# Kernel tuning notes

Measured on AMD Instinct MI355X. Metric: run time of the kernel, lower is better.

## Reference

```python
import jax, jax.numpy as jnp
import numpy as np

IN_CH = 256
OUT_CH = 256
LATENT = 512
SCALE = 1.0 / IN_CH ** 0.5


def setup_inputs() -> dict:
    key = jax.random.key(0)
    k1, k2, k3, k4 = jax.random.split(key, 4)
    return {
        "x": jax.random.normal(k1, (16, IN_CH, 64, 64), dtype=jnp.float32),
        "w": jax.random.normal(k2, (16, LATENT), dtype=jnp.float32),
        "style_w": jax.random.normal(k3, (IN_CH, LATENT), dtype=jnp.float32) * (1.0 / LATENT ** 0.5),
        "style_b": jnp.zeros((IN_CH,), dtype=jnp.float32),
        "weight": jax.random.normal(k4, (1, OUT_CH, IN_CH, 3, 3), dtype=jnp.float32),
    }


def reference(x, w, style_w, style_b, weight):
    b, c, h, ws = x.shape
    # style = Linear(latent -> in_channels), reshaped to [b,1,in,1,1]
    style = (w @ style_w.T + style_b)[:, None, :, None, None]
    wt = weight * SCALE                    # [1, O, I, 3, 3]
    wt = wt * (style + 1.0)                # [b, O, I, 3, 3]
    demod = jax.lax.rsqrt(jnp.sum(wt * wt, axis=(2, 3, 4), keepdims=True) + 1e-8)
    wt = wt * demod
    # grouped conv: fold batch into channels, groups = b
    x2 = x.reshape(1, b * c, h, ws)
    k = wt.reshape(b * OUT_CH, c, 3, 3)
    out = jax.lax.conv_general_dilated(
        x2, k,
        window_strides=(1, 1),
        padding=((1, 1), (1, 1)),
        dimension_numbers=("NCHW", "OIHW", "NCHW"),
        feature_group_count=b,
    )
    return out.reshape(b, OUT_CH, h, ws)
```

## Files before the change

kernel.cpp:

```cpp
#include <hip/hip_runtime.h>
#include <hip/hip_bf16.h>

#define IN_CH 256
#define OUT_CH 256
#define LATENT 512
#define MSCALE (1.0f / 16.0f)

typedef __attribute__((ext_vector_type(8)))  short bf16x8;
typedef __attribute__((ext_vector_type(16))) float f32x16;
typedef unsigned short u16;

__device__ __forceinline__ u16 f2bf(float f) {
  unsigned int x = __float_as_uint(f);
  x += 0x7fffu + ((x >> 16) & 1u);
  return (u16)(x >> 16);
}

__device__ __forceinline__ void gload_lds16(const u16* g, u16* l) {
#if defined(__has_builtin) && __has_builtin(__builtin_amdgcn_global_load_lds)
  __builtin_amdgcn_global_load_lds(
      (const __attribute__((address_space(1))) unsigned int*)g,
      (__attribute__((address_space(3))) unsigned int*)l, 16, 0, 0);
#else
  int lane = __builtin_amdgcn_mbcnt_hi(~0u, __builtin_amdgcn_mbcnt_lo(~0u, 0));
  ((uint4*)l)[lane] = *(const uint4*)g;
#endif
}

__global__ void k_prep(const float* __restrict__ weight, const float* __restrict__ w,
                       const float* __restrict__ sw, const float* __restrict__ sb,
                       float* __restrict__ wsq, u16* __restrict__ wb,
                       float* __restrict__ mod) {
  const int bid = blockIdx.x, tid = threadIdx.x;
  if (bid < 256) {
    const int o = bid, i = tid;
    const float* wp = weight + ((size_t)o * IN_CH + i) * 9;
    float s = 0.f;
#pragma unroll
    for (int t = 0; t < 9; ++t) {
      float v = wp[t];
      s += v * v;
      wb[(((size_t)t * 32 + (i >> 3)) * OUT_CH + o) * 8 + (i & 7)] = f2bf(v);
    }
    wsq[o * IN_CH + i] = s;
  } else {
    __shared__ float ws[LATENT];
    const int b = bid - 256;
    ws[tid] = w[b * LATENT + tid];
    ws[tid + 256] = w[b * LATENT + 256 + tid];
    __syncthreads();
    const float4* sr = (const float4*)(sw + (size_t)tid * LATENT);
    const float4* wr = (const float4*)ws;
    float s = 0.f;
#pragma unroll 8
    for (int l = 0; l < LATENT / 4; ++l) {
      float4 a = sr[l], c = wr[l];
      s += a.x * c.x + a.y * c.y + a.z * c.z + a.w * c.w;
    }
    mod[b * IN_CH + tid] = (1.0f + s + sb[tid]) * MSCALE;
  }
}

__global__ void k_pad(const float* __restrict__ x, const float* __restrict__ mod,
                      const float* __restrict__ wsq, u16* __restrict__ xs,
                      float* __restrict__ demod) {
  const int bid = blockIdx.x;
  const int b = bid / 66, pr = bid - b * 66;
  const int tid = threadIdx.x;
  u16* rowbase = xs + (size_t)((b * 66 + pr) * 32) * 528;

  if (pr == 0 || pr == 65) {
    uint4 z = {0, 0, 0, 0};
    uint4* p = (uint4*)rowbase;
#pragma unroll
    for (int it = 0; it < 9; ++it) {
      int idx = it * 256 + tid;
      if (idx < 2112) p[idx] = z;
    }
    if (pr == 0) {
      __shared__ float m2[IN_CH];
      float m = mod[b * IN_CH + tid];
      m2[tid] = m * m;
      __syncthreads();
      float s = 1e-8f;
      const float4* wr = (const float4*)(wsq + (size_t)tid * IN_CH);
      const float4* mq = (const float4*)m2;
#pragma unroll 4
      for (int i = 0; i < IN_CH / 4; ++i) {
        float4 a = wr[i], c = mq[i];
        s += a.x * c.x + a.y * c.y + a.z * c.z + a.w * c.w;
      }
      demod[b * OUT_CH + tid] = rsqrtf(s);
    }
    return;
  }

  __shared__ float modsh[IN_CH];
  modsh[tid] = mod[b * IN_CH + tid];
  __syncthreads();

  const int w = tid & 63, Gq = tid >> 6;
  const int h = pr - 1;
  const float* xrow = x + ((size_t)b * IN_CH * 64 + (size_t)h) * 64 + w;

  if (tid < 64) {
    bf16x8 z = {};
    *(bf16x8*)(rowbase + ((size_t)(tid >> 1) * 66 + (tid & 1) * 65) * 8) = z;
  }
#pragma unroll
  for (int it = 0; it < 8; ++it) {
    const int G = it * 4 + Gq;
    const float* p = xrow + (size_t)G * 8 * 4096;
    bf16x8 q;
#pragma unroll
    for (int j = 0; j < 8; ++j)
      q[j] = (short)f2bf(p[(size_t)j * 4096] * modsh[G * 8 + j]);
    *(bf16x8*)(rowbase + ((size_t)G * 66 + (w + 1)) * 8) = q;
  }
}

__global__ __launch_bounds__(256, 2)
void k_conv(const u16* __restrict__ xs, const u16* __restrict__ wb,
            const float* __restrict__ demod, float* __restrict__ out) {
  __shared__ __align__(16) u16 xlds[2 * 10 * 2 * 66 * 8];
  __shared__ __align__(16) u16 wlds[2 * 9 * 2 * 64 * 8];

  const int tid = threadIdx.x;
  const int lane = tid & 63;
  const int wid = tid >> 6;
  const int ol = lane & 31;
  const int hi = lane >> 5;

  const int bid = blockIdx.x;
  const int sbid = ((bid & 7) << 6) | (bid >> 3);
  const int otile = (sbid & 3) << 6;
  const int hbase = ((sbid >> 2) & 7) << 3;
  const int b = sbid >> 5;

  const u16* xsb = xs + (size_t)((b * 66 + hbase) * 32) * 528;

  int xoff[5];
#pragma unroll
  for (int it = 0; it < 5; ++it) {
    int q = it * 256 + tid;
    int r = q / 132, rem = q - r * 132;
    int g = rem / 66, c = rem - g * 66;
    xoff[it] = (r * 32 + g) * 528 + c * 8;
  }
  const int xofft = (9 * 32 + 1) * 528 + (26 + tid) * 8;
  int woff[4];
#pragma unroll
  for (int it = 0; it < 4; ++it) {
    int p = it * 256 + tid;
    int t = p >> 7, g = (p >> 6) & 1, o = p & 63;
    woff[it] = ((t * 32 + g) * OUT_CH + otile + o) * 8;
  }
  const int wofft = ((8 * 32 + ((tid >> 6) & 1)) * OUT_CH + otile + (tid & 63)) * 8;

  auto stage = [&](int buf, int ic) {
    const int ibx = ic * 1056;
    const int ibw = ic * 4096;
    u16* xd = xlds + buf * 10560;
#pragma unroll
    for (int it = 0; it < 5; ++it)
      gload_lds16(xsb + xoff[it] + ibx, xd + (size_t)(it * 256 + wid * 64) * 8);
    if (tid < 40)
      gload_lds16(xsb + xofft + ibx, xd + (size_t)(1280 + wid * 64) * 8);
    u16* wd = wlds + buf * 9216;
#pragma unroll
    for (int it = 0; it < 4; ++it)
      gload_lds16(wb + woff[it] + ibw, wd + (size_t)(it * 256 + wid * 64) * 8);
    if (tid < 128)
      gload_lds16(wb + wofft + ibw, wd + (size_t)(1024 + wid * 64) * 8);
  };

  f32x16 acc[2][4] = {};

  stage(0, 0);
  __syncthreads();

  for (int ic = 0; ic < 16; ++ic) {
    const int buf = ic & 1;
    const u16* xp = xlds + buf * 10560;
    const u16* wp = wlds + buf * 9216;

    if (ic < 15) stage(buf ^ 1, ic + 1);

    bf16x8 Xc[2][6];
#pragma unroll
    for (int rr = 0; rr < 2; ++rr)
#pragma unroll
      for (int ch = 0; ch < 2; ++ch)
#pragma unroll
        for (int dw = 0; dw < 3; ++dw) {
          const int r = 2 * wid + 1 + rr;
          const int c = ch * 32 + ol + dw;
          Xc[rr][ch * 3 + dw] = *(const bf16x8*)(xp + (size_t)((r * 2 + hi) * 66 + c) * 8);
        }

    __builtin_amdgcn_s_setprio(1);
#pragma unroll
    for (int dh = 0; dh < 3; ++dh) {
      bf16x8 A0[3], A1[3];
#pragma unroll
      for (int dw = 0; dw < 3; ++dw) {
        const int t = dh * 3 + dw;
        A0[dw] = *(const bf16x8*)(wp + (size_t)((t * 2 + hi) * 64 + ol) * 8);
        A1[dw] = *(const bf16x8*)(wp + (size_t)((t * 2 + hi) * 64 + 32 + ol) * 8);
      }
#pragma unroll
      for (int dw = 0; dw < 3; ++dw) {
#pragma unroll
        for (int ps = 0; ps < 4; ++ps) {
          const int rowoff = ps >> 1, ch = ps & 1;
          const int rl = rowoff + dh;
          bf16x8 B;
          if (rl == 0 || rl == 3) {
            const int r = 2 * wid + rl;
            const int c = ch * 32 + ol + dw;
            B = *(const bf16x8*)(xp + (size_t)((r * 2 + hi) * 66 + c) * 8);
          } else {
            B = Xc[rl - 1][ch * 3 + dw];
          }
          acc[0][ps] = __builtin_amdgcn_mfma_f32_32x32x16_bf16(A0[dw], B, acc[0][ps], 0, 0, 0);
          acc[1][ps] = __builtin_amdgcn_mfma_f32_32x32x16_bf16(A1[dw], B, acc[1][ps], 0, 0, 0);
        }
      }
    }
    __builtin_amdgcn_s_setprio(0);
    __syncthreads();
  }

  const float* dmb = demod + b * OUT_CH + otile;
  float* outb = out + (size_t)b * OUT_CH * 4096;
#pragma unroll
  for (int os = 0; os < 2; ++os) {
    float dm[16];
#pragma unroll
    for (int qd = 0; qd < 4; ++qd) {
      float4 d4 = *(const float4*)(dmb + os * 32 + qd * 8 + hi * 4);
      dm[qd * 4 + 0] = d4.x; dm[qd * 4 + 1] = d4.y;
      dm[qd * 4 + 2] = d4.z; dm[qd * 4 + 3] = d4.w;
    }
#pragma unroll
    for (int ps = 0; ps < 4; ++ps) {
      const int prow = hbase + 2 * wid + (ps >> 1);
      const int col = (ps & 1) * 32 + ol;
#pragma unroll
      for (int rr = 0; rr < 16; ++rr) {
        const int orow = (rr & 3) + 8 * (rr >> 2) + 4 * hi;
        const int o = otile + os * 32 + orow;
        outb[(size_t)o * 4096 + prow * 64 + col] = acc[os][ps][rr] * dm[rr];
      }
    }
  }
}

extern "C" void kernel_launch(void* const* d_in, const int* in_sizes, int n_in,
                              void* d_out, int out_size, void* d_ws, size_t ws_size,
                              hipStream_t stream) {
  const float* x  = (const float*)d_in[0];
  const float* w  = (const float*)d_in[1];
  const float* sw = (const float*)d_in[2];
  const float* sb = (const float*)d_in[3];
  const float* wt = (const float*)d_in[4];
  float* out = (float*)d_out;

  char* ws = (char*)d_ws;
  u16*   xs    = (u16*)(ws);
  u16*   wbuf  = (u16*)(ws + 35684352);
  float* mod   = (float*)(ws + 36864000);
  float* demod = (float*)(ws + 36880384);
  float* wsq   = (float*)(ws + 36896768);
  if (ws_size < 37158912u) return;

  k_prep<<<272, 256, 0, stream>>>(wt, w, sw, sb, wsq, wbuf, mod);
  k_pad <<<16 * 66, 256, 0, stream>>>(x, mod, wsq, xs, demod);
  k_conv<<<512, 256, 0, stream>>>(xs, wbuf, demod, out);
}
```

Baseline: 105.4 us.

## Halve conv tile height, single-buffer X tile, raise occupancy to three blocks

The conv block now covers 4 output rows instead of 8, so there are twice as many blocks. Each warp accumulates one row instead of two, which halves the accumulator registers and drops the cached X rows. The X tile in LDS is single-buffered, staged after a barrier at the end of each iteration, while the weights stay double-buffered. Launch bounds are raised to 3 blocks per SM and demod is cached in LDS. The aim is more resident waves to hide latency, at the cost of less weight reuse per block, more halo reloads, and X loads that are no longer overlapped with compute.

```diff
diff --git a/kernel.cpp b/kernel.cpp
--- a/kernel.cpp
+++ b/kernel.cpp
@@ -119,11 +119,12 @@
   }
 }
 
-__global__ __launch_bounds__(256, 2)
+__global__ __launch_bounds__(256, 3)
 void k_conv(const u16* __restrict__ xs, const u16* __restrict__ wb,
             const float* __restrict__ demod, float* __restrict__ out) {
-  __shared__ __align__(16) u16 xlds[2 * 10 * 2 * 66 * 8];
+  __shared__ __align__(16) u16 xlds[6 * 2 * 66 * 8];
   __shared__ __align__(16) u16 wlds[2 * 9 * 2 * 64 * 8];
+  __shared__ __align__(16) float dmsh[64];
 
   const int tid = threadIdx.x;
   const int lane = tid & 63;
@@ -132,41 +133,47 @@
   const int hi = lane >> 5;
 
   const int bid = blockIdx.x;
-  const int sbid = ((bid & 7) << 6) | (bid >> 3);
+  const int sbid = ((bid & 7) << 7) | (bid >> 3);
   const int otile = (sbid & 3) << 6;
-  const int hbase = ((sbid >> 2) & 7) << 3;
-  const int b = sbid >> 5;
-
-  const u16* xsb = xs + (size_t)((b * 66 + hbase) * 32) * 528;
-
-  int xoff[5];
-#pragma unroll
-  for (int it = 0; it < 5; ++it) {
+  const int hb = ((sbid >> 2) & 15) << 2;
+  const int b = sbid >> 6;
+
+  const u16* xsb = xs + (size_t)((b * 66 + hb) * 32) * 528;
+
+  int xoff[3];
+#pragma unroll
+  for (int it = 0; it < 3; ++it) {
     int q = it * 256 + tid;
     int r = q / 132, rem = q - r * 132;
     int g = rem / 66, c = rem - g * 66;
     xoff[it] = (r * 32 + g) * 528 + c * 8;
   }
-  const int xofft = (9 * 32 + 1) * 528 + (26 + tid) * 8;
+  int xofft;
+  {
+    int q = 768 + tid;
+    int r = q / 132, rem = q - r * 132;
+    int g = rem / 66, c = rem - g * 66;
+    xofft = (r * 32 + g) * 528 + c * 8;
+  }
   int woff[4];
 #pragma unroll
   for (int it = 0; it < 4; ++it) {
-    int p = it * 256 + tid;
-    int t = p >> 7, g = (p >> 6) & 1, o = p & 63;
+    int q = it * 256 + tid;
+    int t = q >> 7, g = (q >> 6) & 1, o = q & 63;
     woff[it] = ((t * 32 + g) * OUT_CH + otile + o) * 8;
   }
   const int wofft = ((8 * 32 + ((tid >> 6) & 1)) * OUT_CH + otile + (tid & 63)) * 8;
 
-  auto stage = [&](int buf, int ic) {
+  auto stageX = [&](int ic) {
     const int ibx = ic * 1056;
+#pragma unroll
+    for (int it = 0; it < 3; ++it)
+      gload_lds16(xsb + xoff[it] + ibx, xlds + (size_t)(it * 256 + wid * 64) * 8);
+    if (tid < 24)
+      gload_lds16(xsb + xofft + ibx, xlds + (size_t)(768 + wid * 64) * 8);
+  };
+  auto stageW = [&](int ic, u16* wd) {
     const int ibw = ic * 4096;
-    u16* xd = xlds + buf * 10560;
-#pragma unroll
-    for (int it = 0; it < 5; ++it)
-      gload_lds16(xsb + xoff[it] + ibx, xd + (size_t)(it * 256 + wid * 64) * 8);
-    if (tid < 40)
-      gload_lds16(xsb + xofft + ibx, xd + (size_t)(1280 + wid * 64) * 8);
-    u16* wd = wlds + buf * 9216;
 #pragma unroll
     for (int it = 0; it < 4; ++it)
       gload_lds16(wb + woff[it] + ibw, wd + (size_t)(it * 256 + wid * 64) * 8);
@@ -174,83 +181,58 @@
       gload_lds16(wb + wofft + ibw, wd + (size_t)(1024 + wid * 64) * 8);
   };
 
-  f32x16 acc[2][4] = {};
-
-  stage(0, 0);
+  f32x16 acc[2][2] = {};
+
+  if (tid < 64) dmsh[tid] = demod[b * OUT_CH + otile + tid];
+  stageX(0);
+  stageW(0, wlds);
   __syncthreads();
 
   for (int ic = 0; ic < 16; ++ic) {
-    const int buf = ic & 1;
-    const u16* xp = xlds + buf * 10560;
-    const u16* wp = wlds + buf * 9216;
-
-    if (ic < 15) stage(buf ^ 1, ic + 1);
-
-    bf16x8 Xc[2][6];
-#pragma unroll
-    for (int rr = 0; rr < 2; ++rr)
-#pragma unroll
-      for (int ch = 0; ch < 2; ++ch)
-#pragma unroll
-        for (int dw = 0; dw < 3; ++dw) {
-          const int r = 2 * wid + 1 + rr;
-          const int c = ch * 32 + ol + dw;
-          Xc[rr][ch * 3 + dw] = *(const bf16x8*)(xp + (size_t)((r * 2 + hi) * 66 + c) * 8);
-        }
+    const u16* wp = wlds + (ic & 1) * 9216;
+    if (ic < 15) stageW(ic + 1, wlds + ((ic & 1) ^ 1) * 9216);
 
     __builtin_amdgcn_s_setprio(1);
 #pragma unroll
-    for (int dh = 0; dh < 3; ++dh) {
-      bf16x8 A0[3], A1[3];
-#pragma unroll
-      for (int dw = 0; dw < 3; ++dw) {
-        const int t = dh * 3 + dw;
-        A0[dw] = *(const bf16x8*)(wp + (size_t)((t * 2 + hi) * 64 + ol) * 8);
-        A1[dw] = *(const bf16x8*)(wp + (size_t)((t * 2 + hi) * 64 + 32 + ol) * 8);
+    for (int t = 0; t < 9; ++t) {
+      const int dh = t / 3, dw = t - dh * 3;
+      bf16x8 A0 = *(const bf16x8*)(wp + (size_t)((t * 2 + hi) * 64 + ol) * 8);
+      bf16x8 A1 = *(const bf16x8*)(wp + (size_t)((t * 2 + hi) * 64 + 32 + ol) * 8);
+#pragma unroll
+      for (int ch = 0; ch < 2; ++ch) {
+        const int rl = wid + dh;
+        const int c = ch * 32 + ol + dw;
+        bf16x8 B = *(const bf16x8*)(xlds + (size_t)((rl * 2 + hi) * 66 + c) * 8);
+        acc[0][ch] = __builtin_amdgcn_mfma_f32_32x32x16_bf16(A0, B, acc[0][ch], 0, 0, 0);
+        acc[1][ch] = __builtin_amdgcn_mfma_f32_32x32x16_bf16(A1, B, acc[1][ch], 0, 0, 0);
       }
-#pragma unroll
-      for (int dw = 0; dw < 3; ++dw) {
-#pragma unroll
-        for (int ps = 0; ps < 4; ++ps) {
-          const int rowoff = ps >> 1, ch = ps & 1;
-          const int rl = rowoff + dh;
-          bf16x8 B;
-          if (rl == 0 || rl == 3) {
-            const int r = 2 * wid + rl;
-            const int c = ch * 32 + ol + dw;
-            B = *(const bf16x8*)(xp + (size_t)((r * 2 + hi) * 66 + c) * 8);
-          } else {
-            B = Xc[rl - 1][ch * 3 + dw];
-          }
-          acc[0][ps] = __builtin_amdgcn_mfma_f32_32x32x16_bf16(A0[dw], B, acc[0][ps], 0, 0, 0);
-          acc[1][ps] = __builtin_amdgcn_mfma_f32_32x32x16_bf16(A1[dw], B, acc[1][ps], 0, 0, 0);
-        }
-      }
     }
     __builtin_amdgcn_s_setprio(0);
+
+    __builtin_amdgcn_s_barrier();
+    if (ic < 15) stageX(ic + 1);
     __syncthreads();
   }
 
-  const float* dmb = demod + b * OUT_CH + otile;
   float* outb = out + (size_t)b * OUT_CH * 4096;
+  const int prow = hb + wid;
 #pragma unroll
   for (int os = 0; os < 2; ++os) {
     float dm[16];
 #pragma unroll
     for (int qd = 0; qd < 4; ++qd) {
-      float4 d4 = *(const float4*)(dmb + os * 32 + qd * 8 + hi * 4);
+      float4 d4 = *(const float4*)(dmsh + os * 32 + qd * 8 + hi * 4);
       dm[qd * 4 + 0] = d4.x; dm[qd * 4 + 1] = d4.y;
       dm[qd * 4 + 2] = d4.z; dm[qd * 4 + 3] = d4.w;
     }
 #pragma unroll
-    for (int ps = 0; ps < 4; ++ps) {
-      const int prow = hbase + 2 * wid + (ps >> 1);
-      const int col = (ps & 1) * 32 + ol;
+    for (int ch = 0; ch < 2; ++ch) {
+      const int col = ch * 32 + ol;
 #pragma unroll
       for (int rr = 0; rr < 16; ++rr) {
         const int orow = (rr & 3) + 8 * (rr >> 2) + 4 * hi;
         const int o = otile + os * 32 + orow;
-        outb[(size_t)o * 4096 + prow * 64 + col] = acc[os][ps][rr] * dm[rr];
+        outb[(size_t)o * 4096 + prow * 64 + col] = acc[os][ch][rr] * dm[rr];
       }
     }
   }
@@ -276,5 +258,5 @@
 
   k_prep<<<272, 256, 0, stream>>>(wt, w, sw, sb, wsq, wbuf, mod);
   k_pad <<<16 * 66, 256, 0, stream>>>(x, mod, wsq, xs, demod);
-  k_conv<<<512, 256, 0, stream>>>(xs, wbuf, demod, out);
-}
+  k_conv<<<1024, 256, 0, stream>>>(xs, wbuf, demod, out);
+}
```

Measured after the change: 115.5 us. 1.1x slower.
